# Optimization experiments

Hardware: AMD Instinct MI355X
Metric: run time of the kernel (lower is better)

Reference implementation:

```python
import jax, jax.numpy as jnp
import numpy as np

N_NODES = 100000


def gcn_conv(x, W, b, src, dst, norm, n_nodes):
    # x: [N, F_in] -> [N, F_out]; GCNConv: D^-1/2 (A+I) D^-1/2 (X W) + b
    h = x @ W                                   # [N, F_out]
    msg = h[src] * norm[:, None]                # [E+N, F_out] gather + scale
    out = jax.ops.segment_sum(msg, dst, num_segments=n_nodes)  # scatter-add
    return out + b


def setup_inputs() -> dict:
    key = jax.random.key(0)
    k0, k1, k2, k3, k4, k5 = jax.random.split(key, 6)
    n, e, f_in, f_hid, n_cls = N_NODES, 1600000, 128, 128, 3
    x = jax.random.normal(k0, (n, f_in), dtype=jnp.float32)
    edge_index = jax.random.randint(k1, (2, e), 0, n, dtype=jnp.int64)
    s1 = 1.0 / np.sqrt(f_in)
    s2 = 1.0 / np.sqrt(f_hid)
    W1 = jax.random.uniform(k2, (f_in, f_hid), jnp.float32, -s1, s1)
    b1 = jnp.zeros((f_hid,), jnp.float32)
    W2 = jax.random.uniform(k3, (f_hid, f_hid), jnp.float32, -s2, s2)
    b2 = jnp.zeros((f_hid,), jnp.float32)
    Wfc = jax.random.uniform(k4, (f_hid, n_cls), jnp.float32, -s2, s2)
    bfc = jax.random.uniform(k5, (n_cls,), jnp.float32, -s2, s2)
    return {"x": x, "edge_index": edge_index, "W1": W1, "b1": b1,
            "W2": W2, "b2": b2, "Wfc": Wfc, "bfc": bfc}


def reference(x, edge_index, W1, b1, W2, b2, Wfc, bfc):
    n = x.shape[0]
    # add self-loops (PyG GCNConv default add_self_loops=True)
    loops = jnp.arange(n, dtype=edge_index.dtype)
    src = jnp.concatenate([edge_index[0], loops])
    dst = jnp.concatenate([edge_index[1], loops])
    deg = jax.ops.segment_sum(jnp.ones_like(dst, dtype=x.dtype), dst,
                              num_segments=n)
    dinv = jax.lax.rsqrt(deg)                   # deg >= 1 due to self-loops
    norm = dinv[src] * dinv[dst]                # [E+N]
    h = jax.nn.relu(gcn_conv(x, W1, b1, src, dst, norm, n))   # dropout=eval id
    h = jax.nn.relu(gcn_conv(h, W2, b2, src, dst, norm, n))
    return jnp.tanh(h @ Wfc + bfc)              # [N, 3]
```

## Files before the change

kernel.cpp:

```cpp
#include <hip/hip_runtime.h>
#include <hip/hip_bf16.h>
#include <hip/hip_fp16.h>


#define NODE_F 128

typedef __attribute__((ext_vector_type(8))) short bf16x8;
typedef __attribute__((ext_vector_type(8))) unsigned short u16x8;
typedef __attribute__((ext_vector_type(4))) float f32x4;

__device__ inline unsigned short bf16_rn(float x) {
    unsigned u = __builtin_bit_cast(unsigned, x);
    unsigned r = (u + 0x7fffu + ((u >> 16) & 1u)) >> 16;
    return (unsigned short)r;
}
__device__ inline float bf16_to_f(unsigned short h) {
    unsigned u = (unsigned)h << 16;
    return __builtin_bit_cast(float, u);
}
__device__ inline void acc8_h(float a[8], uint4 v) {
    unsigned vv[4] = {v.x, v.y, v.z, v.w};
    #pragma unroll
    for (int j = 0; j < 4; ++j) {
        float2 f = __half22float2(__builtin_bit_cast(__half2, vv[j]));
        a[2 * j]     += f.x;
        a[2 * j + 1] += f.y;
    }
}


__global__ __launch_bounds__(256) void wconv_kernel(const float* __restrict__ W1,
                                                    const float* __restrict__ W2,
                                                    unsigned short* __restrict__ WhiT,
                                                    unsigned short* __restrict__ WloT)
{
    const float* W = blockIdx.x ? W2 : W1;
    unsigned short* hiT = WhiT + blockIdx.x * 128 * 128;
    unsigned short* loT = WloT + blockIdx.x * 128 * 128;
    int tid = threadIdx.x;
    for (int i = tid; i < 128 * 128; i += 256) {
        int k = i >> 7, n = i & 127;
        float x = W[i];
        unsigned short hi = bf16_rn(x);
        float lo = x - bf16_to_f(hi);
        hiT[n * 128 + k] = hi;
        loT[n * 128 + k] = bf16_rn(lo);
    }
}


__global__ __launch_bounds__(256) void scan_block_kernel(
    const int* __restrict__ degE, int* __restrict__ row_start,
    int* __restrict__ bsum, int N)
{
    __shared__ int s[256];
    const int tid = threadIdx.x;
    const int idx = blockIdx.x * 1024 + tid * 4;
    int v0 = (idx + 0 < N) ? degE[idx + 0] : 0;
    int v1 = (idx + 1 < N) ? degE[idx + 1] : 0;
    int v2 = (idx + 2 < N) ? degE[idx + 2] : 0;
    int v3 = (idx + 3 < N) ? degE[idx + 3] : 0;
    int t = v0 + v1 + v2 + v3;
    s[tid] = t;
    __syncthreads();
    #pragma unroll
    for (int off = 1; off < 256; off <<= 1) {
        int x = (tid >= off) ? s[tid - off] : 0;
        __syncthreads();
        s[tid] += x;
        __syncthreads();
    }
    int excl = s[tid] - t;
    if (idx + 0 < N) row_start[idx + 0] = excl;
    if (idx + 1 < N) row_start[idx + 1] = excl + v0;
    if (idx + 2 < N) row_start[idx + 2] = excl + v0 + v1;
    if (idx + 3 < N) row_start[idx + 3] = excl + v0 + v1 + v2;
    if (tid == 255) bsum[blockIdx.x] = s[255];
}

__global__ __launch_bounds__(1024) void scan_tops_kernel(int* __restrict__ bsum, int nb) {
    __shared__ int s[1024];
    const int tid = threadIdx.x;
    int v = (tid < nb) ? bsum[tid] : 0;
    s[tid] = v;
    __syncthreads();
    #pragma unroll
    for (int off = 1; off < 1024; off <<= 1) {
        int x = (tid >= off) ? s[tid - off] : 0;
        __syncthreads();
        s[tid] += x;
        __syncthreads();
    }
    if (tid < nb) bsum[tid] = s[tid] - v;
}

__global__ void scan_finish_kernel(const int* __restrict__ degE, int* __restrict__ row_start,
                                   const int* __restrict__ bsum, float* __restrict__ dinv, int N)
{
    int i = blockIdx.x * blockDim.x + threadIdx.x;
    if (i >= N) return;
    int rs = row_start[i] + bsum[i >> 10];
    row_start[i] = rs;
    dinv[i] = rsqrtf((float)degE[i] + 1.0f);
    if (i == N - 1) row_start[N] = rs + degE[i];
}


template<bool SPLIT_IN, bool SCALE_OUT>
__device__ __forceinline__ void gemm_body(
    const float* __restrict__ Xf,
    const unsigned short* __restrict__ Xhi_g, const unsigned short* __restrict__ Xlo_g,
    const unsigned short* __restrict__ WhiT, const unsigned short* __restrict__ WloT,
    const float* __restrict__ dinv,
    __half* __restrict__ Hout, int N, int bid,
    unsigned short* xhi, unsigned short* xlo)
{
    const int tid  = threadIdx.x;
    const int lane = tid & 63;
    const int w    = tid >> 6;
    const int rbase = bid * 64;

    bf16x8 bhi[2][4], blo[2][4];
    {
        int n0   = w * 32 + (lane & 15);
        int koct = (lane >> 4) * 8;
        #pragma unroll
        for (int nt = 0; nt < 2; ++nt) {
            #pragma unroll
            for (int kk = 0; kk < 4; ++kk) {
                size_t o = (size_t)(n0 + nt * 16) * 128 + kk * 32 + koct;
                bhi[nt][kk] = *reinterpret_cast<const bf16x8*>(WhiT + o);
                blo[nt][kk] = *reinterpret_cast<const bf16x8*>(WloT + o);
            }
        }
    }

    if (!SPLIT_IN) {
        #pragma unroll
        for (int it = 0; it < 8; ++it) {
            int f   = it * 256 + tid;
            int row = f >> 5;
            int k4  = f & 31;
            float4 v = make_float4(0.f, 0.f, 0.f, 0.f);
            if (rbase + row < N)
                v = *reinterpret_cast<const float4*>(Xf + (size_t)(rbase + row) * NODE_F + k4 * 4);
            float xs[4] = {v.x, v.y, v.z, v.w};
            ushort4 h4, l4;
            unsigned short* hp = &h4.x;
            unsigned short* lp = &l4.x;
            #pragma unroll
            for (int j = 0; j < 4; ++j) {
                unsigned short hi = bf16_rn(xs[j]);
                hp[j] = hi;
                lp[j] = bf16_rn(xs[j] - bf16_to_f(hi));
            }
            int byte = row * 256 + ((k4 * 8) ^ ((row & 7) << 4));
            *reinterpret_cast<ushort4*>(reinterpret_cast<char*>(xhi) + byte) = h4;
            *reinterpret_cast<ushort4*>(reinterpret_cast<char*>(xlo) + byte) = l4;
        }
    } else {
        #pragma unroll
        for (int it = 0; it < 4; ++it) {
            int idx = it * 256 + tid;
            int row = idx >> 4;
            int k8  = idx & 15;
            u16x8 h = {0, 0, 0, 0, 0, 0, 0, 0};
            u16x8 l = {0, 0, 0, 0, 0, 0, 0, 0};
            if (rbase + row < N) {
                size_t g = (size_t)(rbase + row) * NODE_F + k8 * 8;
                h = *reinterpret_cast<const u16x8*>(Xhi_g + g);
                l = *reinterpret_cast<const u16x8*>(Xlo_g + g);
            }
            int byte = row * 256 + ((k8 * 16) ^ ((row & 7) << 4));
            *reinterpret_cast<u16x8*>(reinterpret_cast<char*>(xhi) + byte) = h;
            *reinterpret_cast<u16x8*>(reinterpret_cast<char*>(xlo) + byte) = l;
        }
    }
    __syncthreads();

    f32x4 acc[4][2];
    #pragma unroll
    for (int m = 0; m < 4; ++m)
        #pragma unroll
        for (int nt = 0; nt < 2; ++nt)
            acc[m][nt] = (f32x4){0.f, 0.f, 0.f, 0.f};

    #pragma unroll
    for (int kk = 0; kk < 4; ++kk) {
        #pragma unroll
        for (int m = 0; m < 4; ++m) {
            int row  = m * 16 + (lane & 15);
            int koff = kk * 64 + (lane >> 4) * 16;
            int byte = row * 256 + (koff ^ ((row & 7) << 4));
            bf16x8 ahi = *reinterpret_cast<const bf16x8*>(reinterpret_cast<char*>(xhi) + byte);
            bf16x8 alo = *reinterpret_cast<const bf16x8*>(reinterpret_cast<char*>(xlo) + byte);
            #pragma unroll
            for (int nt = 0; nt < 2; ++nt) {
                acc[m][nt] = __builtin_amdgcn_mfma_f32_16x16x32_bf16(ahi, bhi[nt][kk], acc[m][nt], 0, 0, 0);
                acc[m][nt] = __builtin_amdgcn_mfma_f32_16x16x32_bf16(ahi, blo[nt][kk], acc[m][nt], 0, 0, 0);
                acc[m][nt] = __builtin_amdgcn_mfma_f32_16x16x32_bf16(alo, bhi[nt][kk], acc[m][nt], 0, 0, 0);
            }
        }
    }

    #pragma unroll
    for (int m = 0; m < 4; ++m) {
        int row = rbase + m * 16 + (lane >> 4) * 4;
        int col = w * 32 + (lane & 15);
        #pragma unroll
        for (int nt = 0; nt < 2; ++nt) {
            #pragma unroll
            for (int r = 0; r < 4; ++r) {
                if (row + r < N) {
                    float v = acc[m][nt][r];
                    if (SCALE_OUT) v *= dinv[row + r];
                    Hout[(size_t)(row + r) * NODE_F + col + nt * 16] = __float2half(v);
                }
            }
        }
    }
}


__global__ __launch_bounds__(256) void gemm1deg_kernel(
    const int* __restrict__ dst, int* __restrict__ degE, int* __restrict__ rank, int E,
    int edge_blocks, int gemm_blocks,
    const float* __restrict__ X, const unsigned short* __restrict__ WhiT,
    const unsigned short* __restrict__ WloT, __half* __restrict__ H, int N)
{
    __shared__ unsigned short xhi[64 * 128];
    __shared__ unsigned short xlo[64 * 128];
    int q = blockIdx.x / 5, r = blockIdx.x % 5;
    if (r == 4) {
        int stride = edge_blocks * 256;
        for (int e = q * 256 + threadIdx.x; e < E; e += stride)
            rank[e] = atomicAdd(&degE[dst[e]], 1);
    } else {
        int gid = q * 4 + r;
        if (gid < gemm_blocks)
            gemm_body<false, false>(X, nullptr, nullptr, WhiT, WloT, nullptr,
                                    H, N, gid, xhi, xlo);
    }
}


__global__ __launch_bounds__(256) void hybridB_kernel(
    const int* __restrict__ src, const int* __restrict__ dst,
    const int* __restrict__ rank, const int* __restrict__ row_start,
    int* __restrict__ csr_src, int E, int fill_blocks,
    __half* __restrict__ H, const int* __restrict__ degE, int N)
{
    if ((int)blockIdx.x < fill_blocks) {
        int e = blockIdx.x * 256 + threadIdx.x;
        if (e < E) csr_src[row_start[dst[e]] + rank[e]] = src[e];
    } else {
        int idx = (blockIdx.x - fill_blocks) * 256 + threadIdx.x;
        if (idx < N * 16) {
            int row = idx >> 4;
            float ds = rsqrtf((float)degE[row] + 1.0f);
            __half2* p = reinterpret_cast<__half2*>(H) + (size_t)idx * 4;
            #pragma unroll
            for (int j = 0; j < 4; ++j) {
                float2 v = __half22float2(p[j]);
                v.x *= ds; v.y *= ds;
                p[j] = __float22half2_rn(v);
            }
        }
    }
}


__device__ __forceinline__ void gather_core(
    const __half* __restrict__ Hs, const int* __restrict__ csr_src,
    const int* __restrict__ row_start, int node, int ql, int qi, float a[8])
{
    const char* Hb = reinterpret_cast<const char*>(Hs);
    #pragma unroll
    for (int j = 0; j < 8; ++j) a[j] = 0.f;
    if (qi == 0)
        acc8_h(a, *reinterpret_cast<const uint4*>(Hb + ((size_t)node * 256 + ql * 16)));

    int i   = row_start[node];
    int end = row_start[node + 1];
    for (; i + 7 < end; i += 8) {
        int s0 = csr_src[i + qi];
        int s1 = csr_src[i + 4 + qi];
        uint4 v0 = *reinterpret_cast<const uint4*>(Hb + ((size_t)s0 * 256 + ql * 16));
        uint4 v1 = *reinterpret_cast<const uint4*>(Hb + ((size_t)s1 * 256 + ql * 16));
        acc8_h(a, v0);
        acc8_h(a, v1);
    }
    for (; i < end; i += 4) {
        if (i + qi < end) {
            int s = csr_src[i + qi];
            acc8_h(a, *reinterpret_cast<const uint4*>(Hb + ((size_t)s * 256 + ql * 16)));
        }
    }
    #pragma unroll
    for (int j = 0; j < 8; ++j) {
        a[j] += __shfl_xor(a[j], 32);
        a[j] += __shfl_xor(a[j], 16);
    }
}


__global__ __launch_bounds__(256) void gather1_kernel(
    const __half* __restrict__ Hs, const int* __restrict__ csr_src,
    const int* __restrict__ row_start, const float* __restrict__ dinv,
    const float* __restrict__ b,
    unsigned short* __restrict__ Xhi, unsigned short* __restrict__ Xlo, int N)
{
    int node = (blockIdx.x * blockDim.x + threadIdx.x) >> 6;
    int lane = threadIdx.x & 63;
    int ql = lane & 15, qi = lane >> 4;
    if (node >= N) return;

    float a[8];
    gather_core(Hs, csr_src, row_start, node, ql, qi, a);

    if (qi == 0) {
        const float dd = dinv[node];
        u16x8 h8, l8;
        #pragma unroll
        for (int j = 0; j < 8; ++j) {
            float r = fmaxf(b[ql * 8 + j] + dd * a[j], 0.f);
            unsigned short hi = bf16_rn(r);
            h8[j] = hi;
            l8[j] = bf16_rn(r - bf16_to_f(hi));
        }
        *reinterpret_cast<u16x8*>(Xhi + (size_t)node * NODE_F + ql * 8) = h8;
        *reinterpret_cast<u16x8*>(Xlo + (size_t)node * NODE_F + ql * 8) = l8;
    }
}


__global__ __launch_bounds__(256) void gather2fc_kernel(
    const __half* __restrict__ Hs, const int* __restrict__ csr_src,
    const int* __restrict__ row_start, const float* __restrict__ dinv,
    const float* __restrict__ b, const float* __restrict__ Wfc,
    const float* __restrict__ bfc, float* __restrict__ out, int N)
{
    int node = (blockIdx.x * blockDim.x + threadIdx.x) >> 6;
    int lane = threadIdx.x & 63;
    int ql = lane & 15, qi = lane >> 4;
    if (node >= N) return;

    float a[8];
    gather_core(Hs, csr_src, row_start, node, ql, qi, a);

    const float dd = dinv[node];
    float p0 = 0.f, p1 = 0.f, p2 = 0.f;
    #pragma unroll
    for (int j = 0; j < 8; ++j) {
        float r = fmaxf(b[ql * 8 + j] + dd * a[j], 0.f);
        const float* wr = Wfc + (size_t)(ql * 8 + j) * 3;
        p0 += r * wr[0]; p1 += r * wr[1]; p2 += r * wr[2];
    }
    #pragma unroll
    for (int off = 8; off > 0; off >>= 1) {
        p0 += __shfl_down(p0, off);
        p1 += __shfl_down(p1, off);
        p2 += __shfl_down(p2, off);
    }
    if (lane == 0) {
        out[(size_t)node * 3 + 0] = tanhf(p0 + bfc[0]);
        out[(size_t)node * 3 + 1] = tanhf(p1 + bfc[1]);
        out[(size_t)node * 3 + 2] = tanhf(p2 + bfc[2]);
    }
}


__global__ __launch_bounds__(256) void gemm2_kernel(
    const unsigned short* __restrict__ Xhi_g, const unsigned short* __restrict__ Xlo_g,
    const unsigned short* __restrict__ WhiT, const unsigned short* __restrict__ WloT,
    const float* __restrict__ dinv, __half* __restrict__ Hs, int N)
{
    __shared__ unsigned short xhi[64 * 128];
    __shared__ unsigned short xlo[64 * 128];
    gemm_body<true, true>(nullptr, Xhi_g, Xlo_g, WhiT, WloT, dinv,
                          Hs, N, blockIdx.x, xhi, xlo);
}

extern "C" void kernel_launch(void* const* d_in, const int* in_sizes, int n_in,
                              void* d_out, int out_size, void* d_ws, size_t ws_size,
                              hipStream_t stream)
{
    const float* x    = (const float*)d_in[0];
    const int*   edge = (const int*)d_in[1];
    const float* W1   = (const float*)d_in[2];
    const float* b1   = (const float*)d_in[3];
    const float* W2   = (const float*)d_in[4];
    const float* b2   = (const float*)d_in[5];
    const float* Wfc  = (const float*)d_in[6];
    const float* bfc  = (const float*)d_in[7];
    float* out = (float*)d_out;

    const int N = in_sizes[0] / NODE_F;
    const int E = in_sizes[1] / 2;
    const int* src = edge;
    const int* dst = edge + E;

    char* ws = (char*)d_ws;
    size_t off = 0;
    auto alloc = [&](size_t bytes) {
        void* p = ws + off;
        off += (bytes + 511) & ~511ull;
        return p;
    };
    const int nblk1024 = (N + 1023) / 1024;
    float* dinv      = (float*)alloc((size_t)N * 4);
    int*   degE      = (int*)  alloc((size_t)N * 4);
    int*   rank      = (int*)  alloc((size_t)E * 4);
    int*   row_start = (int*)  alloc((size_t)(N + 1) * 4);
    int*   bsum      = (int*)  alloc((size_t)nblk1024 * 4);
    int*   csr_src   = (int*)  alloc((size_t)E * 4);
    unsigned short* WhiT = (unsigned short*)alloc(2 * 128 * 128 * 2);
    unsigned short* WloT = (unsigned short*)alloc(2 * 128 * 128 * 2);
    __half* Hs       = (__half*)alloc((size_t)N * NODE_F * 2);
    unsigned short* Xhi = (unsigned short*)alloc((size_t)N * NODE_F * 2);
    unsigned short* Xlo = (unsigned short*)alloc((size_t)N * NODE_F * 2);
    (void)ws_size; (void)n_in; (void)out_size;

    const int B = 256;
    const int gemm_grid   = (N + 63) / 64;
    const int edge_grid   = (E + B - 1) / B;
    const int scale_grid  = (N * 16 + B - 1) / B;
    const int gather_grid = (N + 3) / 4;

    const int edge_blocks  = (gemm_grid + 3) / 4;
    const int total_blocks = gemm_grid + edge_blocks + 4;

    wconv_kernel<<<2, B, 0, stream>>>(W1, W2, WhiT, WloT);
    hipMemsetAsync(degE, 0, (size_t)N * 4, stream);

    gemm1deg_kernel<<<total_blocks, B, 0, stream>>>(
        dst, degE, rank, E, edge_blocks, gemm_grid, x, WhiT, WloT, Hs, N);

    scan_block_kernel<<<nblk1024, B, 0, stream>>>(degE, row_start, bsum, N);
    scan_tops_kernel<<<1, 1024, 0, stream>>>(bsum, nblk1024);
    scan_finish_kernel<<<(N + B - 1) / B, B, 0, stream>>>(degE, row_start, bsum, dinv, N);

    hybridB_kernel<<<edge_grid + scale_grid, B, 0, stream>>>(
        src, dst, rank, row_start, csr_src, E, edge_grid, Hs, degE, N);

    gather1_kernel<<<gather_grid, B, 0, stream>>>(Hs, csr_src, row_start, dinv, b1, Xhi, Xlo, N);

    gemm2_kernel<<<gemm_grid, B, 0, stream>>>(Xhi, Xlo, WhiT + 128 * 128, WloT + 128 * 128,
                                              dinv, Hs, N);

    gather2fc_kernel<<<gather_grid, B, 0, stream>>>(Hs, csr_src, row_start, dinv, b2,
                                                    Wfc, bfc, out, N);
}
```

Baseline: 320.8 us.

## Fuse degree count, GEMM1, scan and CSR fill into one cooperative kernel

```diff
diff --git a/kernel.cpp b/kernel.cpp
--- a/kernel.cpp
+++ b/kernel.cpp
@@ -1,6 +1,9 @@
 #include <hip/hip_runtime.h>
 #include <hip/hip_bf16.h>
 #include <hip/hip_fp16.h>
+#include <hip/hip_cooperative_groups.h>
+
+namespace cg = cooperative_groups;
 
 
 #define NODE_F 128
@@ -18,13 +21,13 @@
     unsigned u = (unsigned)h << 16;
     return __builtin_bit_cast(float, u);
 }
-__device__ inline void acc8_h(float a[8], uint4 v) {
+__device__ inline void acc8_h(float a[8], uint4 v, float s) {
     unsigned vv[4] = {v.x, v.y, v.z, v.w};
     #pragma unroll
     for (int j = 0; j < 4; ++j) {
         float2 f = __half22float2(__builtin_bit_cast(__half2, vv[j]));
-        a[2 * j]     += f.x;
-        a[2 * j + 1] += f.y;
+        a[2 * j]     += f.x * s;
+        a[2 * j + 1] += f.y * s;
     }
 }
 
@@ -32,8 +35,10 @@
 __global__ __launch_bounds__(256) void wconv_kernel(const float* __restrict__ W1,
                                                     const float* __restrict__ W2,
                                                     unsigned short* __restrict__ WhiT,
-                                                    unsigned short* __restrict__ WloT)
-{
+                                                    unsigned short* __restrict__ WloT,
+                                                    int* __restrict__ counter)
+{
+    if (blockIdx.x == 0 && threadIdx.x == 0) *counter = 0;
     const float* W = blockIdx.x ? W2 : W1;
     unsigned short* hiT = WhiT + blockIdx.x * 128 * 128;
     unsigned short* loT = WloT + blockIdx.x * 128 * 128;
@@ -46,63 +51,6 @@
         hiT[n * 128 + k] = hi;
         loT[n * 128 + k] = bf16_rn(lo);
     }
-}
-
-
-__global__ __launch_bounds__(256) void scan_block_kernel(
-    const int* __restrict__ degE, int* __restrict__ row_start,
-    int* __restrict__ bsum, int N)
-{
-    __shared__ int s[256];
-    const int tid = threadIdx.x;
-    const int idx = blockIdx.x * 1024 + tid * 4;
-    int v0 = (idx + 0 < N) ? degE[idx + 0] : 0;
-    int v1 = (idx + 1 < N) ? degE[idx + 1] : 0;
-    int v2 = (idx + 2 < N) ? degE[idx + 2] : 0;
-    int v3 = (idx + 3 < N) ? degE[idx + 3] : 0;
-    int t = v0 + v1 + v2 + v3;
-    s[tid] = t;
-    __syncthreads();
-    #pragma unroll
-    for (int off = 1; off < 256; off <<= 1) {
-        int x = (tid >= off) ? s[tid - off] : 0;
-        __syncthreads();
-        s[tid] += x;
-        __syncthreads();
-    }
-    int excl = s[tid] - t;
-    if (idx + 0 < N) row_start[idx + 0] = excl;
-    if (idx + 1 < N) row_start[idx + 1] = excl + v0;
-    if (idx + 2 < N) row_start[idx + 2] = excl + v0 + v1;
-    if (idx + 3 < N) row_start[idx + 3] = excl + v0 + v1 + v2;
-    if (tid == 255) bsum[blockIdx.x] = s[255];
-}
-
-__global__ __launch_bounds__(1024) void scan_tops_kernel(int* __restrict__ bsum, int nb) {
-    __shared__ int s[1024];
-    const int tid = threadIdx.x;
-    int v = (tid < nb) ? bsum[tid] : 0;
-    s[tid] = v;
-    __syncthreads();
-    #pragma unroll
-    for (int off = 1; off < 1024; off <<= 1) {
-        int x = (tid >= off) ? s[tid - off] : 0;
-        __syncthreads();
-        s[tid] += x;
-        __syncthreads();
-    }
-    if (tid < nb) bsum[tid] = s[tid] - v;
-}
-
-__global__ void scan_finish_kernel(const int* __restrict__ degE, int* __restrict__ row_start,
-                                   const int* __restrict__ bsum, float* __restrict__ dinv, int N)
-{
-    int i = blockIdx.x * blockDim.x + threadIdx.x;
-    if (i >= N) return;
-    int rs = row_start[i] + bsum[i >> 10];
-    row_start[i] = rs;
-    dinv[i] = rsqrtf((float)degE[i] + 1.0f);
-    if (i == N - 1) row_start[N] = rs + degE[i];
 }
 
 
@@ -222,78 +170,132 @@
 }
 
 
-__global__ __launch_bounds__(256) void gemm1deg_kernel(
-    const int* __restrict__ dst, int* __restrict__ degE, int* __restrict__ rank, int E,
-    int edge_blocks, int gemm_blocks,
-    const float* __restrict__ X, const unsigned short* __restrict__ WhiT,
-    const unsigned short* __restrict__ WloT, __half* __restrict__ H, int N)
-{
+struct FrontArgs {
+    const int* dst; const int* src;
+    int* degE; unsigned short* rank;
+    int E, N, edge_blocks, gemm_tiles, nblk;
+    const float* X; const unsigned short* WhiT; const unsigned short* WloT;
+    __half* H;
+    int* rsA; int* bsum; int* rsB; float* dinv;
+    int* csr_src; int* counter;
+};
+
+__global__ __launch_bounds__(256) void frontend_kernel(FrontArgs a)
+{
+    cg::grid_group grid = cg::this_grid();
     __shared__ unsigned short xhi[64 * 128];
     __shared__ unsigned short xlo[64 * 128];
-    int q = blockIdx.x / 5, r = blockIdx.x % 5;
-    if (r == 4) {
-        int stride = edge_blocks * 256;
-        for (int e = q * 256 + threadIdx.x; e < E; e += stride)
-            rank[e] = atomicAdd(&degE[dst[e]], 1);
-    } else {
-        int gid = q * 4 + r;
-        if (gid < gemm_blocks)
-            gemm_body<false, false>(X, nullptr, nullptr, WhiT, WloT, nullptr,
-                                    H, N, gid, xhi, xlo);
-    }
-}
-
-
-__global__ __launch_bounds__(256) void hybridB_kernel(
-    const int* __restrict__ src, const int* __restrict__ dst,
-    const int* __restrict__ rank, const int* __restrict__ row_start,
-    int* __restrict__ csr_src, int E, int fill_blocks,
-    __half* __restrict__ H, const int* __restrict__ degE, int N)
-{
-    if ((int)blockIdx.x < fill_blocks) {
-        int e = blockIdx.x * 256 + threadIdx.x;
-        if (e < E) csr_src[row_start[dst[e]] + rank[e]] = src[e];
-    } else {
-        int idx = (blockIdx.x - fill_blocks) * 256 + threadIdx.x;
-        if (idx < N * 16) {
-            int row = idx >> 4;
-            float ds = rsqrtf((float)degE[row] + 1.0f);
-            __half2* p = reinterpret_cast<__half2*>(H) + (size_t)idx * 4;
-            #pragma unroll
-            for (int j = 0; j < 4; ++j) {
-                float2 v = __half22float2(p[j]);
-                v.x *= ds; v.y *= ds;
-                p[j] = __float22half2_rn(v);
-            }
-        }
-    }
-}
-
-
+    const int G   = gridDim.x;
+    const int bid = blockIdx.x;
+    const int tid = threadIdx.x;
+    int* t_sp = reinterpret_cast<int*>(xhi);
+
+    if (bid < a.edge_blocks) {
+        int stride = a.edge_blocks * 256;
+        for (int e = bid * 256 + tid; e < a.E; e += stride)
+            a.rank[e] = (unsigned short)atomicAdd(&a.degE[a.dst[e]], 1);
+    }
+    for (;;) {
+        __syncthreads();
+        if (tid == 0) *t_sp = atomicAdd(a.counter, 1);
+        __syncthreads();
+        int t = *t_sp;
+        __syncthreads();
+        if (t >= a.gemm_tiles) break;
+        gemm_body<false, false>(a.X, nullptr, nullptr, a.WhiT, a.WloT, nullptr,
+                                a.H, a.N, t, xhi, xlo);
+    }
+    grid.sync();
+
+    if (bid < a.nblk) {
+        int* s = reinterpret_cast<int*>(xhi);
+        const int idx = bid * 1024 + tid * 4;
+        int v0 = (idx + 0 < a.N) ? a.degE[idx + 0] : 0;
+        int v1 = (idx + 1 < a.N) ? a.degE[idx + 1] : 0;
+        int v2 = (idx + 2 < a.N) ? a.degE[idx + 2] : 0;
+        int v3 = (idx + 3 < a.N) ? a.degE[idx + 3] : 0;
+        int t = v0 + v1 + v2 + v3;
+        s[tid] = t;
+        __syncthreads();
+        #pragma unroll
+        for (int off = 1; off < 256; off <<= 1) {
+            int x = (tid >= off) ? s[tid - off] : 0;
+            __syncthreads();
+            s[tid] += x;
+            __syncthreads();
+        }
+        int excl = s[tid] - t;
+        if (idx + 0 < a.N) a.rsA[idx + 0] = excl;
+        if (idx + 1 < a.N) a.rsA[idx + 1] = excl + v0;
+        if (idx + 2 < a.N) a.rsA[idx + 2] = excl + v0 + v1;
+        if (idx + 3 < a.N) a.rsA[idx + 3] = excl + v0 + v1 + v2;
+        if (tid == 255) a.bsum[bid] = s[255];
+    }
+    grid.sync();
+
+    if (bid == 0) {
+        int* s = reinterpret_cast<int*>(xhi);
+        int v = (tid < a.nblk) ? a.bsum[tid] : 0;
+        if (tid < 128) s[tid] = v;
+        __syncthreads();
+        #pragma unroll
+        for (int off = 1; off < 128; off <<= 1) {
+            int x = (tid >= off && tid < 128) ? s[tid - off] : 0;
+            __syncthreads();
+            if (tid < 128) s[tid] += x;
+            __syncthreads();
+        }
+        if (tid < a.nblk) a.bsum[tid] = s[tid] - v;
+    }
+    grid.sync();
+
+    {
+        int stride = G * 256;
+        for (int i = bid * 256 + tid; i < a.N; i += stride) {
+            int rs = a.rsA[i] + a.bsum[i >> 10];
+            a.rsB[i] = rs;
+            a.dinv[i] = rsqrtf((float)a.degE[i] + 1.0f);
+            if (i == a.N - 1) a.rsB[a.N] = rs + a.degE[i];
+        }
+        for (int e = bid * 256 + tid; e < a.E; e += stride) {
+            int d = a.dst[e];
+            a.csr_src[a.rsA[d] + a.bsum[d >> 10] + (int)a.rank[e]] = a.src[e];
+        }
+    }
+}
+
+
+template<bool EDGE_SCALE>
 __device__ __forceinline__ void gather_core(
     const __half* __restrict__ Hs, const int* __restrict__ csr_src,
-    const int* __restrict__ row_start, int node, int ql, int qi, float a[8])
+    const int* __restrict__ row_start, const float* __restrict__ dinv,
+    int node, int ql, int qi, float a[8])
 {
     const char* Hb = reinterpret_cast<const char*>(Hs);
     #pragma unroll
     for (int j = 0; j < 8; ++j) a[j] = 0.f;
-    if (qi == 0)
-        acc8_h(a, *reinterpret_cast<const uint4*>(Hb + ((size_t)node * 256 + ql * 16)));
+    if (qi == 0) {
+        float ds = EDGE_SCALE ? dinv[node] : 1.0f;
+        acc8_h(a, *reinterpret_cast<const uint4*>(Hb + ((size_t)node * 256 + ql * 16)), ds);
+    }
 
     int i   = row_start[node];
     int end = row_start[node + 1];
     for (; i + 7 < end; i += 8) {
         int s0 = csr_src[i + qi];
         int s1 = csr_src[i + 4 + qi];
+        float d0 = EDGE_SCALE ? dinv[s0] : 1.0f;
+        float d1 = EDGE_SCALE ? dinv[s1] : 1.0f;
         uint4 v0 = *reinterpret_cast<const uint4*>(Hb + ((size_t)s0 * 256 + ql * 16));
         uint4 v1 = *reinterpret_cast<const uint4*>(Hb + ((size_t)s1 * 256 + ql * 16));
-        acc8_h(a, v0);
-        acc8_h(a, v1);
+        acc8_h(a, v0, d0);
+        acc8_h(a, v1, d1);
     }
     for (; i < end; i += 4) {
         if (i + qi < end) {
             int s = csr_src[i + qi];
-            acc8_h(a, *reinterpret_cast<const uint4*>(Hb + ((size_t)s * 256 + ql * 16)));
+            float ds = EDGE_SCALE ? dinv[s] : 1.0f;
+            acc8_h(a, *reinterpret_cast<const uint4*>(Hb + ((size_t)s * 256 + ql * 16)), ds);
         }
     }
     #pragma unroll
@@ -305,7 +307,7 @@
 
 
 __global__ __launch_bounds__(256) void gather1_kernel(
-    const __half* __restrict__ Hs, const int* __restrict__ csr_src,
+    const __half* __restrict__ H, const int* __restrict__ csr_src,
     const int* __restrict__ row_start, const float* __restrict__ dinv,
     const float* __restrict__ b,
     unsigned short* __restrict__ Xhi, unsigned short* __restrict__ Xlo, int N)
@@ -316,7 +318,7 @@
     if (node >= N) return;
 
     float a[8];
-    gather_core(Hs, csr_src, row_start, node, ql, qi, a);
+    gather_core<true>(H, csr_src, row_start, dinv, node, ql, qi, a);
 
     if (qi == 0) {
         const float dd = dinv[node];
@@ -346,7 +348,7 @@
     if (node >= N) return;
 
     float a[8];
-    gather_core(Hs, csr_src, row_start, node, ql, qi, a);
+    gather_core<false>(Hs, csr_src, row_start, dinv, node, ql, qi, a);
 
     const float dd = dinv[node];
     float p0 = 0.f, p1 = 0.f, p2 = 0.f;
@@ -407,47 +409,57 @@
         off += (bytes + 511) & ~511ull;
         return p;
     };
-    const int nblk1024 = (N + 1023) / 1024;
+    const int nblk = (N + 1023) / 1024;
     float* dinv      = (float*)alloc((size_t)N * 4);
     int*   degE      = (int*)  alloc((size_t)N * 4);
-    int*   rank      = (int*)  alloc((size_t)E * 4);
-    int*   row_start = (int*)  alloc((size_t)(N + 1) * 4);
-    int*   bsum      = (int*)  alloc((size_t)nblk1024 * 4);
+    unsigned short* rank = (unsigned short*)alloc((size_t)E * 2);
+    int*   rsA       = (int*)  alloc((size_t)N * 4);
+    int*   rsB       = (int*)  alloc((size_t)(N + 1) * 4);
+    int*   bsum      = (int*)  alloc((size_t)nblk * 4);
     int*   csr_src   = (int*)  alloc((size_t)E * 4);
+    int*   counter   = (int*)  alloc(4);
     unsigned short* WhiT = (unsigned short*)alloc(2 * 128 * 128 * 2);
     unsigned short* WloT = (unsigned short*)alloc(2 * 128 * 128 * 2);
-    __half* Hs       = (__half*)alloc((size_t)N * NODE_F * 2);
+    __half* H        = (__half*)alloc((size_t)N * NODE_F * 2);
     unsigned short* Xhi = (unsigned short*)alloc((size_t)N * NODE_F * 2);
     unsigned short* Xlo = (unsigned short*)alloc((size_t)N * NODE_F * 2);
     (void)ws_size; (void)n_in; (void)out_size;
 
     const int B = 256;
     const int gemm_grid   = (N + 63) / 64;
-    const int edge_grid   = (E + B - 1) / B;
-    const int scale_grid  = (N * 16 + B - 1) / B;
     const int gather_grid = (N + 3) / 4;
 
-    const int edge_blocks  = (gemm_grid + 3) / 4;
-    const int total_blocks = gemm_grid + edge_blocks + 4;
-
-    wconv_kernel<<<2, B, 0, stream>>>(W1, W2, WhiT, WloT);
+    int dev = 0;
+    hipGetDevice(&dev);
+    hipDeviceProp_t prop;
+    hipGetDeviceProperties(&prop, dev);
+    int bpc = 0;
+    hipOccupancyMaxActiveBlocksPerMultiprocessor(&bpc, frontend_kernel, B, 0);
+    if (bpc <= 0) bpc = 4;
+    int G = prop.multiProcessorCount * bpc;
+    if (G < 256) G = 256;
+    int edge_blocks = G / 4;
+
+    wconv_kernel<<<2, B, 0, stream>>>(W1, W2, WhiT, WloT, counter);
     hipMemsetAsync(degE, 0, (size_t)N * 4, stream);
 
-    gemm1deg_kernel<<<total_blocks, B, 0, stream>>>(
-        dst, degE, rank, E, edge_blocks, gemm_grid, x, WhiT, WloT, Hs, N);
-
-    scan_block_kernel<<<nblk1024, B, 0, stream>>>(degE, row_start, bsum, N);
-    scan_tops_kernel<<<1, 1024, 0, stream>>>(bsum, nblk1024);
-    scan_finish_kernel<<<(N + B - 1) / B, B, 0, stream>>>(degE, row_start, bsum, dinv, N);
-
-    hybridB_kernel<<<edge_grid + scale_grid, B, 0, stream>>>(
-        src, dst, rank, row_start, csr_src, E, edge_grid, Hs, degE, N);
-
-    gather1_kernel<<<gather_grid, B, 0, stream>>>(Hs, csr_src, row_start, dinv, b1, Xhi, Xlo, N);
+    FrontArgs fa;
+    fa.dst = dst; fa.src = src;
+    fa.degE = degE; fa.rank = rank;
+    fa.E = E; fa.N = N; fa.edge_blocks = edge_blocks;
+    fa.gemm_tiles = gemm_grid; fa.nblk = nblk;
+    fa.X = x; fa.WhiT = WhiT; fa.WloT = WloT;
+    fa.H = H;
+    fa.rsA = rsA; fa.bsum = bsum; fa.rsB = rsB; fa.dinv = dinv;
+    fa.csr_src = csr_src; fa.counter = counter;
+    void* kargs[] = {(void*)&fa};
+    hipLaunchCooperativeKernel((void*)frontend_kernel, dim3(G), dim3(B), kargs, 0, stream);
+
+    gather1_kernel<<<gather_grid, B, 0, stream>>>(H, csr_src, rsB, dinv, b1, Xhi, Xlo, N);
 
     gemm2_kernel<<<gemm_grid, B, 0, stream>>>(Xhi, Xlo, WhiT + 128 * 128, WloT + 128 * 128,
-                                              dinv, Hs, N);
-
-    gather2fc_kernel<<<gather_grid, B, 0, stream>>>(Hs, csr_src, row_start, dinv, b2,
+                                              dinv, H, N);
+
+    gather2fc_kernel<<<gather_grid, B, 0, stream>>>(H, csr_src, rsB, dinv, b2,
                                                     Wfc, bfc, out, N);
 }
```

Measured after the change: 420.4 us. 1.31x slower.

## Fuse layer-1 gather into GEMM2, merge scan finish with CSR fill

Applied to the files above, without the earlier changes.

```diff
diff --git a/kernel.cpp b/kernel.cpp
--- a/kernel.cpp
+++ b/kernel.cpp
@@ -18,13 +18,13 @@
     unsigned u = (unsigned)h << 16;
     return __builtin_bit_cast(float, u);
 }
-__device__ inline void acc8_h(float a[8], uint4 v) {
+__device__ inline void acc8_h(float a[8], uint4 v, float s) {
     unsigned vv[4] = {v.x, v.y, v.z, v.w};
     #pragma unroll
     for (int j = 0; j < 4; ++j) {
         float2 f = __half22float2(__builtin_bit_cast(__half2, vv[j]));
-        a[2 * j]     += f.x;
-        a[2 * j + 1] += f.y;
+        a[2 * j]     += f.x * s;
+        a[2 * j + 1] += f.y * s;
     }
 }
 
@@ -50,7 +50,7 @@
 
 
 __global__ __launch_bounds__(256) void scan_block_kernel(
-    const int* __restrict__ degE, int* __restrict__ row_start,
+    const int* __restrict__ degE, int* __restrict__ rsA,
     int* __restrict__ bsum, int N)
 {
     __shared__ int s[256];
@@ -71,10 +71,10 @@
         __syncthreads();
     }
     int excl = s[tid] - t;
-    if (idx + 0 < N) row_start[idx + 0] = excl;
-    if (idx + 1 < N) row_start[idx + 1] = excl + v0;
-    if (idx + 2 < N) row_start[idx + 2] = excl + v0 + v1;
-    if (idx + 3 < N) row_start[idx + 3] = excl + v0 + v1 + v2;
+    if (idx + 0 < N) rsA[idx + 0] = excl;
+    if (idx + 1 < N) rsA[idx + 1] = excl + v0;
+    if (idx + 2 < N) rsA[idx + 2] = excl + v0 + v1;
+    if (idx + 3 < N) rsA[idx + 3] = excl + v0 + v1 + v2;
     if (tid == 255) bsum[blockIdx.x] = s[255];
 }
 
@@ -94,31 +94,42 @@
     if (tid < nb) bsum[tid] = s[tid] - v;
 }
 
-__global__ void scan_finish_kernel(const int* __restrict__ degE, int* __restrict__ row_start,
-                                   const int* __restrict__ bsum, float* __restrict__ dinv, int N)
-{
-    int i = blockIdx.x * blockDim.x + threadIdx.x;
-    if (i >= N) return;
-    int rs = row_start[i] + bsum[i >> 10];
-    row_start[i] = rs;
-    dinv[i] = rsqrtf((float)degE[i] + 1.0f);
-    if (i == N - 1) row_start[N] = rs + degE[i];
-}
-
-
-template<bool SPLIT_IN, bool SCALE_OUT>
-__device__ __forceinline__ void gemm_body(
-    const float* __restrict__ Xf,
-    const unsigned short* __restrict__ Xhi_g, const unsigned short* __restrict__ Xlo_g,
+
+__global__ __launch_bounds__(256) void finish_fill_kernel(
+    const int* __restrict__ src, const int* __restrict__ dst,
+    const unsigned short* __restrict__ rank,
+    const int* __restrict__ rsA, const int* __restrict__ bsum,
+    int* __restrict__ rsB, float* __restrict__ dinv,
+    const int* __restrict__ degE, int* __restrict__ csr_src,
+    int E, int N, int fill_blocks)
+{
+    if ((int)blockIdx.x < fill_blocks) {
+        int e = blockIdx.x * 256 + threadIdx.x;
+        if (e < E) {
+            int d = dst[e];
+            csr_src[rsA[d] + bsum[d >> 10] + (int)rank[e]] = src[e];
+        }
+    } else {
+        int i = (blockIdx.x - fill_blocks) * 256 + threadIdx.x;
+        if (i < N) {
+            int rs = rsA[i] + bsum[i >> 10];
+            rsB[i] = rs;
+            dinv[i] = rsqrtf((float)degE[i] + 1.0f);
+            if (i == N - 1) rsB[N] = rs + degE[i];
+        }
+    }
+}
+
+
+template<bool SCALE_OUT>
+__device__ __forceinline__ void gemm_compute(
     const unsigned short* __restrict__ WhiT, const unsigned short* __restrict__ WloT,
-    const float* __restrict__ dinv,
-    __half* __restrict__ Hout, int N, int bid,
+    const float* __restrict__ dinv, __half* __restrict__ Hout, int N, int rbase,
     unsigned short* xhi, unsigned short* xlo)
 {
     const int tid  = threadIdx.x;
     const int lane = tid & 63;
     const int w    = tid >> 6;
-    const int rbase = bid * 64;
 
     bf16x8 bhi[2][4], blo[2][4];
     {
@@ -134,49 +145,6 @@
             }
         }
     }
-
-    if (!SPLIT_IN) {
-        #pragma unroll
-        for (int it = 0; it < 8; ++it) {
-            int f   = it * 256 + tid;
-            int row = f >> 5;
-            int k4  = f & 31;
-            float4 v = make_float4(0.f, 0.f, 0.f, 0.f);
-            if (rbase + row < N)
-                v = *reinterpret_cast<const float4*>(Xf + (size_t)(rbase + row) * NODE_F + k4 * 4);
-            float xs[4] = {v.x, v.y, v.z, v.w};
-            ushort4 h4, l4;
-            unsigned short* hp = &h4.x;
-            unsigned short* lp = &l4.x;
-            #pragma unroll
-            for (int j = 0; j < 4; ++j) {
-                unsigned short hi = bf16_rn(xs[j]);
-                hp[j] = hi;
-                lp[j] = bf16_rn(xs[j] - bf16_to_f(hi));
-            }
-            int byte = row * 256 + ((k4 * 8) ^ ((row & 7) << 4));
-            *reinterpret_cast<ushort4*>(reinterpret_cast<char*>(xhi) + byte) = h4;
-            *reinterpret_cast<ushort4*>(reinterpret_cast<char*>(xlo) + byte) = l4;
-        }
-    } else {
-        #pragma unroll
-        for (int it = 0; it < 4; ++it) {
-            int idx = it * 256 + tid;
-            int row = idx >> 4;
-            int k8  = idx & 15;
-            u16x8 h = {0, 0, 0, 0, 0, 0, 0, 0};
-            u16x8 l = {0, 0, 0, 0, 0, 0, 0, 0};
-            if (rbase + row < N) {
-                size_t g = (size_t)(rbase + row) * NODE_F + k8 * 8;
-                h = *reinterpret_cast<const u16x8*>(Xhi_g + g);
-                l = *reinterpret_cast<const u16x8*>(Xlo_g + g);
-            }
-            int byte = row * 256 + ((k8 * 16) ^ ((row & 7) << 4));
-            *reinterpret_cast<u16x8*>(reinterpret_cast<char*>(xhi) + byte) = h;
-            *reinterpret_cast<u16x8*>(reinterpret_cast<char*>(xlo) + byte) = l;
-        }
-    }
-    __syncthreads();
 
     f32x4 acc[4][2];
     #pragma unroll
@@ -222,8 +190,45 @@
 }
 
 
+__device__ __forceinline__ void gemm1_body(
+    const float* __restrict__ Xf,
+    const unsigned short* __restrict__ WhiT, const unsigned short* __restrict__ WloT,
+    __half* __restrict__ Hout, int N, int bid,
+    unsigned short* xhi, unsigned short* xlo)
+{
+    const int tid   = threadIdx.x;
+    const int rbase = bid * 64;
+
+    #pragma unroll
+    for (int it = 0; it < 8; ++it) {
+        int f   = it * 256 + tid;
+        int row = f >> 5;
+        int k4  = f & 31;
+        float4 v = make_float4(0.f, 0.f, 0.f, 0.f);
+        if (rbase + row < N)
+            v = *reinterpret_cast<const float4*>(Xf + (size_t)(rbase + row) * NODE_F + k4 * 4);
+        float xs[4] = {v.x, v.y, v.z, v.w};
+        ushort4 h4, l4;
+        unsigned short* hp = &h4.x;
+        unsigned short* lp = &l4.x;
+        #pragma unroll
+        for (int j = 0; j < 4; ++j) {
+            unsigned short hi = bf16_rn(xs[j]);
+            hp[j] = hi;
+            lp[j] = bf16_rn(xs[j] - bf16_to_f(hi));
+        }
+        int byte = row * 256 + ((k4 * 8) ^ ((row & 7) << 4));
+        *reinterpret_cast<ushort4*>(reinterpret_cast<char*>(xhi) + byte) = h4;
+        *reinterpret_cast<ushort4*>(reinterpret_cast<char*>(xlo) + byte) = l4;
+    }
+    __syncthreads();
+    gemm_compute<false>(WhiT, WloT, nullptr, Hout, N, rbase, xhi, xlo);
+}
+
+
 __global__ __launch_bounds__(256) void gemm1deg_kernel(
-    const int* __restrict__ dst, int* __restrict__ degE, int* __restrict__ rank, int E,
+    const int* __restrict__ dst, int* __restrict__ degE,
+    unsigned short* __restrict__ rank, int E,
     int edge_blocks, int gemm_blocks,
     const float* __restrict__ X, const unsigned short* __restrict__ WhiT,
     const unsigned short* __restrict__ WloT, __half* __restrict__ H, int N)
@@ -234,66 +239,46 @@
     if (r == 4) {
         int stride = edge_blocks * 256;
         for (int e = q * 256 + threadIdx.x; e < E; e += stride)
-            rank[e] = atomicAdd(&degE[dst[e]], 1);
+            rank[e] = (unsigned short)atomicAdd(&degE[dst[e]], 1);
     } else {
         int gid = q * 4 + r;
         if (gid < gemm_blocks)
-            gemm_body<false, false>(X, nullptr, nullptr, WhiT, WloT, nullptr,
-                                    H, N, gid, xhi, xlo);
-    }
-}
-
-
-__global__ __launch_bounds__(256) void hybridB_kernel(
-    const int* __restrict__ src, const int* __restrict__ dst,
-    const int* __restrict__ rank, const int* __restrict__ row_start,
-    int* __restrict__ csr_src, int E, int fill_blocks,
-    __half* __restrict__ H, const int* __restrict__ degE, int N)
-{
-    if ((int)blockIdx.x < fill_blocks) {
-        int e = blockIdx.x * 256 + threadIdx.x;
-        if (e < E) csr_src[row_start[dst[e]] + rank[e]] = src[e];
-    } else {
-        int idx = (blockIdx.x - fill_blocks) * 256 + threadIdx.x;
-        if (idx < N * 16) {
-            int row = idx >> 4;
-            float ds = rsqrtf((float)degE[row] + 1.0f);
-            __half2* p = reinterpret_cast<__half2*>(H) + (size_t)idx * 4;
-            #pragma unroll
-            for (int j = 0; j < 4; ++j) {
-                float2 v = __half22float2(p[j]);
-                v.x *= ds; v.y *= ds;
-                p[j] = __float22half2_rn(v);
-            }
-        }
-    }
-}
-
-
+            gemm1_body(X, WhiT, WloT, H, N, gid, xhi, xlo);
+    }
+}
+
+
+template<bool EDGE_SCALE>
 __device__ __forceinline__ void gather_core(
     const __half* __restrict__ Hs, const int* __restrict__ csr_src,
-    const int* __restrict__ row_start, int node, int ql, int qi, float a[8])
+    const int* __restrict__ row_start, const float* __restrict__ dinv,
+    int node, int ql, int qi, float a[8])
 {
     const char* Hb = reinterpret_cast<const char*>(Hs);
     #pragma unroll
     for (int j = 0; j < 8; ++j) a[j] = 0.f;
-    if (qi == 0)
-        acc8_h(a, *reinterpret_cast<const uint4*>(Hb + ((size_t)node * 256 + ql * 16)));
+    if (qi == 0) {
+        float ds = EDGE_SCALE ? dinv[node] : 1.0f;
+        acc8_h(a, *reinterpret_cast<const uint4*>(Hb + ((size_t)node * 256 + ql * 16)), ds);
+    }
 
     int i   = row_start[node];
     int end = row_start[node + 1];
     for (; i + 7 < end; i += 8) {
         int s0 = csr_src[i + qi];
         int s1 = csr_src[i + 4 + qi];
+        float d0 = EDGE_SCALE ? dinv[s0] : 1.0f;
+        float d1 = EDGE_SCALE ? dinv[s1] : 1.0f;
         uint4 v0 = *reinterpret_cast<const uint4*>(Hb + ((size_t)s0 * 256 + ql * 16));
         uint4 v1 = *reinterpret_cast<const uint4*>(Hb + ((size_t)s1 * 256 + ql * 16));
-        acc8_h(a, v0);
-        acc8_h(a, v1);
+        acc8_h(a, v0, d0);
+        acc8_h(a, v1, d1);
     }
     for (; i < end; i += 4) {
         if (i + qi < end) {
             int s = csr_src[i + qi];
-            acc8_h(a, *reinterpret_cast<const uint4*>(Hb + ((size_t)s * 256 + ql * 16)));
+            float ds = EDGE_SCALE ? dinv[s] : 1.0f;
+            acc8_h(a, *reinterpret_cast<const uint4*>(Hb + ((size_t)s * 256 + ql * 16)), ds);
         }
     }
     #pragma unroll
@@ -304,33 +289,55 @@
 }
 
 
-__global__ __launch_bounds__(256) void gather1_kernel(
-    const __half* __restrict__ Hs, const int* __restrict__ csr_src,
+__global__ __launch_bounds__(256) void aggemm2_kernel(
+    const __half* __restrict__ H, const int* __restrict__ csr_src,
     const int* __restrict__ row_start, const float* __restrict__ dinv,
-    const float* __restrict__ b,
-    unsigned short* __restrict__ Xhi, unsigned short* __restrict__ Xlo, int N)
-{
-    int node = (blockIdx.x * blockDim.x + threadIdx.x) >> 6;
-    int lane = threadIdx.x & 63;
-    int ql = lane & 15, qi = lane >> 4;
-    if (node >= N) return;
-
-    float a[8];
-    gather_core(Hs, csr_src, row_start, node, ql, qi, a);
-
-    if (qi == 0) {
-        const float dd = dinv[node];
-        u16x8 h8, l8;
-        #pragma unroll
-        for (int j = 0; j < 8; ++j) {
-            float r = fmaxf(b[ql * 8 + j] + dd * a[j], 0.f);
-            unsigned short hi = bf16_rn(r);
-            h8[j] = hi;
-            l8[j] = bf16_rn(r - bf16_to_f(hi));
-        }
-        *reinterpret_cast<u16x8*>(Xhi + (size_t)node * NODE_F + ql * 8) = h8;
-        *reinterpret_cast<u16x8*>(Xlo + (size_t)node * NODE_F + ql * 8) = l8;
-    }
+    const float* __restrict__ b1,
+    const unsigned short* __restrict__ WhiT, const unsigned short* __restrict__ WloT,
+    __half* __restrict__ H2, int N)
+{
+    __shared__ unsigned short xhi[64 * 128];
+    __shared__ unsigned short xlo[64 * 128];
+    const int tid  = threadIdx.x;
+    const int lane = tid & 63;
+    const int w    = tid >> 6;
+    const int ql   = lane & 15, qi = lane >> 4;
+    const int rbase = blockIdx.x * 64;
+
+    float bv[8];
+    {
+        float4 b0 = *reinterpret_cast<const float4*>(b1 + ql * 8);
+        float4 b4 = *reinterpret_cast<const float4*>(b1 + ql * 8 + 4);
+        bv[0] = b0.x; bv[1] = b0.y; bv[2] = b0.z; bv[3] = b0.w;
+        bv[4] = b4.x; bv[5] = b4.y; bv[6] = b4.z; bv[7] = b4.w;
+    }
+
+    for (int r16 = 0; r16 < 16; ++r16) {
+        int row  = w * 16 + r16;
+        int node = rbase + row;
+        float a[8];
+        if (node < N)
+            gather_core<true>(H, csr_src, row_start, dinv, node, ql, qi, a);
+        if (qi == 0) {
+            u16x8 h8 = {0, 0, 0, 0, 0, 0, 0, 0};
+            u16x8 l8 = {0, 0, 0, 0, 0, 0, 0, 0};
+            if (node < N) {
+                float dd = dinv[node];
+                #pragma unroll
+                for (int j = 0; j < 8; ++j) {
+                    float r = fmaxf(bv[j] + dd * a[j], 0.f);
+                    unsigned short hi = bf16_rn(r);
+                    h8[j] = hi;
+                    l8[j] = bf16_rn(r - bf16_to_f(hi));
+                }
+            }
+            int byte = row * 256 + ((ql * 16) ^ ((row & 7) << 4));
+            *reinterpret_cast<u16x8*>(reinterpret_cast<char*>(xhi) + byte) = h8;
+            *reinterpret_cast<u16x8*>(reinterpret_cast<char*>(xlo) + byte) = l8;
+        }
+    }
+    __syncthreads();
+    gemm_compute<true>(WhiT, WloT, dinv, H2, N, rbase, xhi, xlo);
 }
 
 
@@ -346,7 +353,7 @@
     if (node >= N) return;
 
     float a[8];
-    gather_core(Hs, csr_src, row_start, node, ql, qi, a);
+    gather_core<false>(Hs, csr_src, row_start, dinv, node, ql, qi, a);
 
     const float dd = dinv[node];
     float p0 = 0.f, p1 = 0.f, p2 = 0.f;
@@ -367,18 +374,6 @@
         out[(size_t)node * 3 + 1] = tanhf(p1 + bfc[1]);
         out[(size_t)node * 3 + 2] = tanhf(p2 + bfc[2]);
     }
-}
-
-
-__global__ __launch_bounds__(256) void gemm2_kernel(
-    const unsigned short* __restrict__ Xhi_g, const unsigned short* __restrict__ Xlo_g,
-    const unsigned short* __restrict__ WhiT, const unsigned short* __restrict__ WloT,
-    const float* __restrict__ dinv, __half* __restrict__ Hs, int N)
-{
-    __shared__ unsigned short xhi[64 * 128];
-    __shared__ unsigned short xlo[64 * 128];
-    gemm_body<true, true>(nullptr, Xhi_g, Xlo_g, WhiT, WloT, dinv,
-                          Hs, N, blockIdx.x, xhi, xlo);
 }
 
 extern "C" void kernel_launch(void* const* d_in, const int* in_sizes, int n_in,
@@ -407,25 +402,25 @@
         off += (bytes + 511) & ~511ull;
         return p;
     };
-    const int nblk1024 = (N + 1023) / 1024;
+    const int nblk = (N + 1023) / 1024;
     float* dinv      = (float*)alloc((size_t)N * 4);
     int*   degE      = (int*)  alloc((size_t)N * 4);
-    int*   rank      = (int*)  alloc((size_t)E * 4);
-    int*   row_start = (int*)  alloc((size_t)(N + 1) * 4);
-    int*   bsum      = (int*)  alloc((size_t)nblk1024 * 4);
+    unsigned short* rank = (unsigned short*)alloc((size_t)E * 2);
+    int*   rsA       = (int*)  alloc((size_t)N * 4);
+    int*   rsB       = (int*)  alloc((size_t)(N + 1) * 4);
+    int*   bsum      = (int*)  alloc((size_t)nblk * 4);
     int*   csr_src   = (int*)  alloc((size_t)E * 4);
     unsigned short* WhiT = (unsigned short*)alloc(2 * 128 * 128 * 2);
     unsigned short* WloT = (unsigned short*)alloc(2 * 128 * 128 * 2);
-    __half* Hs       = (__half*)alloc((size_t)N * NODE_F * 2);
-    unsigned short* Xhi = (unsigned short*)alloc((size_t)N * NODE_F * 2);
-    unsigned short* Xlo = (unsigned short*)alloc((size_t)N * NODE_F * 2);
+    __half* H        = (__half*)alloc((size_t)N * NODE_F * 2);
+    __half* H2       = (__half*)alloc((size_t)N * NODE_F * 2);
     (void)ws_size; (void)n_in; (void)out_size;
 
     const int B = 256;
     const int gemm_grid   = (N + 63) / 64;
-    const int edge_grid   = (E + B - 1) / B;
-    const int scale_grid  = (N * 16 + B - 1) / B;
     const int gather_grid = (N + 3) / 4;
+    const int fill_blocks = (E + B - 1) / B;
+    const int fin_blocks  = (N + B - 1) / B;
 
     const int edge_blocks  = (gemm_grid + 3) / 4;
     const int total_blocks = gemm_grid + edge_blocks + 4;
@@ -434,20 +429,17 @@
     hipMemsetAsync(degE, 0, (size_t)N * 4, stream);
 
     gemm1deg_kernel<<<total_blocks, B, 0, stream>>>(
-        dst, degE, rank, E, edge_blocks, gemm_grid, x, WhiT, WloT, Hs, N);
-
-    scan_block_kernel<<<nblk1024, B, 0, stream>>>(degE, row_start, bsum, N);
-    scan_tops_kernel<<<1, 1024, 0, stream>>>(bsum, nblk1024);
-    scan_finish_kernel<<<(N + B - 1) / B, B, 0, stream>>>(degE, row_start, bsum, dinv, N);
-
-    hybridB_kernel<<<edge_grid + scale_grid, B, 0, stream>>>(
-        src, dst, rank, row_start, csr_src, E, edge_grid, Hs, degE, N);
-
-    gather1_kernel<<<gather_grid, B, 0, stream>>>(Hs, csr_src, row_start, dinv, b1, Xhi, Xlo, N);
-
-    gemm2_kernel<<<gemm_grid, B, 0, stream>>>(Xhi, Xlo, WhiT + 128 * 128, WloT + 128 * 128,
-                                              dinv, Hs, N);
-
-    gather2fc_kernel<<<gather_grid, B, 0, stream>>>(Hs, csr_src, row_start, dinv, b2,
+        dst, degE, rank, E, edge_blocks, gemm_grid, x, WhiT, WloT, H, N);
+
+    scan_block_kernel<<<nblk, B, 0, stream>>>(degE, rsA, bsum, N);
+    scan_tops_kernel<<<1, 1024, 0, stream>>>(bsum, nblk);
+
+    finish_fill_kernel<<<fill_blocks + fin_blocks, B, 0, stream>>>(
+        src, dst, rank, rsA, bsum, rsB, dinv, degE, csr_src, E, N, fill_blocks);
+
+    aggemm2_kernel<<<gemm_grid, B, 0, stream>>>(
+        H, csr_src, rsB, dinv, b1, WhiT + 128 * 128, WloT + 128 * 128, H2, N);
+
+    gather2fc_kernel<<<gather_grid, B, 0, stream>>>(H2, csr_src, rsB, dinv, b2,
                                                     Wfc, bfc, out, N);
 }
```

Measured after the change: 340.5 us. 6.1% more time.
